# Performance work log

Measured on AMD Instinct MI355X. Metric: run time of the kernel, lower is better.

## Reference

```python
import jax, jax.numpy as jnp
import numpy as np
import math

B, N, D, K = 4, 4096, 1024, 8


def setup_inputs() -> dict:
    key = jax.random.key(0)
    ks = jax.random.split(key, 9)
    s = 0.02
    return {
        "summaries": jax.random.normal(ks[0], (B, N, D), dtype=jnp.float32),
        "Wq": jax.random.normal(ks[1], (D, D), dtype=jnp.float32) * s,
        "bq": jnp.zeros((D,), dtype=jnp.float32),
        "Wk": jax.random.normal(ks[2], (D, D), dtype=jnp.float32) * s,
        "bk": jnp.zeros((D,), dtype=jnp.float32),
        "Wv": jax.random.normal(ks[3], (D, D), dtype=jnp.float32) * s,
        "bv": jnp.zeros((D,), dtype=jnp.float32),
        "Wo": jax.random.normal(ks[4], (D, D), dtype=jnp.float32) * s,
        "bo": jnp.zeros((D,), dtype=jnp.float32),
    }


def reference(summaries, Wq, bq, Wk, bk, Wv, bv, Wo, bo):
    b_, n_, d_ = summaries.shape
    q = summaries @ Wq + bq
    k = summaries @ Wk + bk
    v = summaries @ Wv + bv
    # [B, N, N] causal scores
    scores = jnp.einsum("bnd,bmd->bnm", q, k) / math.sqrt(d_)
    causal = jnp.triu(jnp.full((n_, n_), -jnp.inf, dtype=scores.dtype), k=1)
    scores = scores + causal
    # top-k sparse attention (N > K here, matching the torch branch)
    topk_vals, topk_idx = jax.lax.top_k(scores, K)  # [B, N, K]
    bi = jnp.arange(b_)[:, None, None]
    ri = jnp.arange(n_)[None, :, None]
    sparse = jnp.full_like(scores, -jnp.inf).at[bi, ri, topk_idx].set(topk_vals)
    attn = jax.nn.softmax(sparse, axis=-1)
    out = jnp.einsum("bnm,bmd->bnd", attn, v)
    return out @ Wo + bo
```

## Files before the change

### kernel.cpp

```cpp
#include <hip/hip_runtime.h>
#include <cstdint>
#include <cstddef>

#define B_ 4
#define N_ 4096
#define D_ 1024
#define CAND 16
#define M_ (B_*N_)
#define MD_ ((size_t)M_ * D_)
#define DD_ ((size_t)D_ * D_)

typedef __attribute__((ext_vector_type(8))) short short8;
typedef __attribute__((ext_vector_type(4))) float floatx4;

__device__ __align__(16) float          g_Qf[MD_];
__device__ __align__(16) float          g_Kf[MD_];
__device__ __align__(16) unsigned short g_Qb[MD_];
__device__ __align__(16) unsigned short g_Kb[MD_];
__device__ __align__(16) float          g_Vf[MD_];
__device__ __align__(16) unsigned short g_AO[MD_];
__device__ __align__(16) unsigned short g_X0[MD_];
__device__ __align__(16) unsigned short g_X1[MD_];
__device__ __align__(16) unsigned short g_Wq0T[DD_];
__device__ __align__(16) unsigned short g_Wq1T[DD_];
__device__ __align__(16) unsigned short g_Wk0T[DD_];
__device__ __align__(16) unsigned short g_Wk1T[DD_];
__device__ __align__(16) unsigned short g_WvT[DD_];
__device__ __align__(16) unsigned short g_WoT[DD_];
__device__ __align__(16) float          g_S[(size_t)B_ * N_ * N_];
__device__ __align__(16) int            g_cand[(size_t)M_ * CAND];

__device__ __forceinline__ float b2f(unsigned short u){
  return __uint_as_float(((unsigned int)u) << 16);
}
__device__ __forceinline__ unsigned short f2b(float f){
  unsigned int b = __float_as_uint(f);
  b += 0x7fffu + ((b >> 16) & 1u);
  return (unsigned short)(b >> 16);
}
__device__ __forceinline__ void split2(float x, unsigned short& h0,
                                       unsigned short& h1){
  h0 = f2b(x);
  float r1 = x - b2f(h0);
  h1 = f2b(r1);
}

__device__ __forceinline__ void gl_lds16(const void* g, void* l){
  __builtin_amdgcn_global_load_lds(
      (const __attribute__((address_space(1))) unsigned int*)g,
      (__attribute__((address_space(3))) unsigned int*)l, 16, 0, 0);
}

__global__ __launch_bounds__(256)
void transpose2(const float* __restrict__ Wv, const float* __restrict__ Wo){
  __shared__ float tile[32][33];
  const float* src = blockIdx.z ? Wo : Wv;
  unsigned short* dst = blockIdx.z ? g_WoT : g_WvT;
  int tx = threadIdx.x, ty = threadIdx.y;
  int n0 = blockIdx.x * 32, k0 = blockIdx.y * 32;
  for (int r = ty; r < 32; r += 8) tile[r][tx] = src[(size_t)(k0 + r) * D_ + n0 + tx];
  __syncthreads();
  for (int r = ty; r < 32; r += 8) dst[(size_t)(n0 + r) * D_ + k0 + tx] = f2b(tile[tx][r]);
}

__global__ __launch_bounds__(256)
void split_wT(const float* __restrict__ Wq, const float* __restrict__ Wk){
  __shared__ float tile[32][33];
  const float* src = blockIdx.z ? Wk : Wq;
  unsigned short* d0 = blockIdx.z ? g_Wk0T : g_Wq0T;
  unsigned short* d1 = blockIdx.z ? g_Wk1T : g_Wq1T;
  int tx = threadIdx.x, ty = threadIdx.y;
  int n0 = blockIdx.x * 32, k0 = blockIdx.y * 32;
  for (int r = ty; r < 32; r += 8) tile[r][tx] = src[(size_t)(k0 + r) * D_ + n0 + tx];
  __syncthreads();
  for (int r = ty; r < 32; r += 8){
    unsigned short h0, h1;
    split2(tile[tx][r], h0, h1);
    size_t o = (size_t)(n0 + r) * D_ + k0 + tx;
    d0[o] = h0; d1[o] = h1;
  }
}

__global__ __launch_bounds__(256)
void split_x(const float* __restrict__ X){
  size_t i = ((size_t)blockIdx.x * 256 + threadIdx.x) * 4;
  if (i >= MD_) return;
  float4 x = *(const float4*)&X[i];
  ushort4 u0, u1;
  split2(x.x, u0.x, u1.x);
  split2(x.y, u0.y, u1.y);
  split2(x.z, u0.z, u1.z);
  split2(x.w, u0.w, u1.w);
  *(ushort4*)&g_X0[i] = u0;
  *(ushort4*)&g_X1[i] = u1;
}

__global__ __launch_bounds__(256, 2)
void qk_split_gemm(const float* __restrict__ bias, int which){
  int p = blockIdx.x;
  int lin = (p & 7) * 128 + (p >> 3);
  int mt = lin >> 3;
  int nt = lin & 7;

  const unsigned short* __restrict__ B0 = which ? g_Wk0T : g_Wq0T;
  const unsigned short* __restrict__ B1 = which ? g_Wk1T : g_Wq1T;
  float* __restrict__ outf = which ? g_Kf : g_Qf;
  unsigned short* __restrict__ outb = which ? g_Kb : g_Qb;

  __shared__ unsigned short __align__(16) As0[128 * 64];
  __shared__ unsigned short __align__(16) As1[128 * 64];
  __shared__ unsigned short __align__(16) Bs0[128 * 64];
  __shared__ unsigned short __align__(16) Bs1[128 * 64];

  int tid = threadIdx.x;
  size_t m0 = (size_t)mt * 128;
  int n0 = nt * 128;
  int l = tid & 63, wid = tid >> 6;
  int wm = (wid >> 1) * 64, wn = (wid & 1) * 64;
  int quad = l >> 4, lr = l & 15;

  floatx4 acc[4][4];
  #pragma unroll
  for (int i = 0; i < 4; i++)
    #pragma unroll
    for (int j = 0; j < 4; j++) acc[i][j] = (floatx4)0.0f;

  for (int k0 = 0; k0 < D_; k0 += 64){
    #pragma unroll
    for (int c = 0; c < 4; c++){
      int d = c * 4096 + tid * 16;
      int rw = d >> 7;
      int sc = ((d & 127) ^ ((rw & 7) << 4)) >> 1;
      size_t ao = (m0 + rw) * D_ + k0 + sc;
      size_t bo = (size_t)(n0 + rw) * D_ + k0 + sc;
      gl_lds16(&g_X0[ao], &As0[d >> 1]);
      gl_lds16(&g_X1[ao], &As1[d >> 1]);
      gl_lds16(&B0[bo], &Bs0[d >> 1]);
      gl_lds16(&B1[bo], &Bs1[d >> 1]);
    }
    __syncthreads();
    #pragma unroll
    for (int kk = 0; kk < 2; kk++){
      short8 a0[4], a1[4], b0[4], b1[4];
      #pragma unroll
      for (int i = 0; i < 4; i++){
        int rw = wm + i * 16 + lr;
        int byt = rw * 128 + ((kk * 64 + quad * 16) ^ ((rw & 7) << 4));
        a0[i] = *(const short8*)&As0[byt >> 1];
        a1[i] = *(const short8*)&As1[byt >> 1];
      }
      #pragma unroll
      for (int j = 0; j < 4; j++){
        int rw = wn + j * 16 + lr;
        int byt = rw * 128 + ((kk * 64 + quad * 16) ^ ((rw & 7) << 4));
        b0[j] = *(const short8*)&Bs0[byt >> 1];
        b1[j] = *(const short8*)&Bs1[byt >> 1];
      }
      #pragma unroll
      for (int i = 0; i < 4; i++)
        #pragma unroll
        for (int j = 0; j < 4; j++){
          acc[i][j] = __builtin_amdgcn_mfma_f32_16x16x32_bf16(a0[i], b1[j], acc[i][j], 0, 0, 0);
          acc[i][j] = __builtin_amdgcn_mfma_f32_16x16x32_bf16(a1[i], b0[j], acc[i][j], 0, 0, 0);
          acc[i][j] = __builtin_amdgcn_mfma_f32_16x16x32_bf16(a0[i], b0[j], acc[i][j], 0, 0, 0);
        }
    }
    __syncthreads();
  }
  #pragma unroll
  for (int i = 0; i < 4; i++)
    #pragma unroll
    for (int j = 0; j < 4; j++)
      #pragma unroll
      for (int rg = 0; rg < 4; rg++){
        size_t row = m0 + wm + i * 16 + quad * 4 + rg;
        int col = n0 + wn + j * 16 + lr;
        float val = acc[i][j][rg] + bias[col];
        outf[row * D_ + col] = val;
        outb[row * D_ + col] = f2b(val);
      }
}

__global__ __launch_bounds__(256, 2)
void gemm_bf16(const float* __restrict__ bias, float* __restrict__ Cout, int sel){
  const unsigned short* Asrc = sel ? g_AO : g_X0;
  const unsigned short* Bt = sel ? g_WoT : g_WvT;
  float* C = sel ? Cout : g_Vf;
  __shared__ unsigned short __align__(16) As[128 * 128];
  __shared__ unsigned short __align__(16) Bs[128 * 128];
  int p = blockIdx.x;
  int lin = (p & 7) * 128 + (p >> 3);
  int mt = lin >> 3;
  int nt = lin & 7;
  int tid = threadIdx.x;
  size_t m0 = (size_t)mt * 128;
  int n0 = nt * 128;
  int l = tid & 63, wid = tid >> 6;
  int wm = (wid >> 1) * 64, wn = (wid & 1) * 64;
  int quad = l >> 4, lr = l & 15;
  floatx4 acc[4][4];
  #pragma unroll
  for (int i = 0; i < 4; i++)
    #pragma unroll
    for (int j = 0; j < 4; j++) acc[i][j] = (floatx4)0.0f;

  for (int k0 = 0; k0 < D_; k0 += 128){
    #pragma unroll
    for (int c = 0; c < 8; c++){
      int d = c * 4096 + tid * 16;
      int rw = d >> 8;
      int sc = ((d & 255) ^ ((rw & 7) << 4)) >> 1;
      gl_lds16(&Asrc[(m0 + rw) * D_ + k0 + sc], &As[d >> 1]);
      gl_lds16(&Bt[(size_t)(n0 + rw) * D_ + k0 + sc], &Bs[d >> 1]);
    }
    __syncthreads();
    #pragma unroll
    for (int kk = 0; kk < 4; kk++){
      short8 af[4], bf[4];
      #pragma unroll
      for (int i = 0; i < 4; i++){
        int rw = wm + i * 16 + lr;
        int byt = rw * 256 + ((kk * 64 + quad * 16) ^ ((rw & 7) << 4));
        af[i] = *(const short8*)&As[byt >> 1];
      }
      #pragma unroll
      for (int j = 0; j < 4; j++){
        int rw = wn + j * 16 + lr;
        int byt = rw * 256 + ((kk * 64 + quad * 16) ^ ((rw & 7) << 4));
        bf[j] = *(const short8*)&Bs[byt >> 1];
      }
      #pragma unroll
      for (int i = 0; i < 4; i++)
        #pragma unroll
        for (int j = 0; j < 4; j++)
          acc[i][j] = __builtin_amdgcn_mfma_f32_16x16x32_bf16(af[i], bf[j], acc[i][j], 0, 0, 0);
    }
    __syncthreads();
  }
  #pragma unroll
  for (int i = 0; i < 4; i++)
    #pragma unroll
    for (int j = 0; j < 4; j++)
      #pragma unroll
      for (int rg = 0; rg < 4; rg++){
        size_t row = m0 + wm + i * 16 + quad * 4 + rg;
        int col = n0 + wn + j * 16 + lr;
        C[row * D_ + col] = acc[i][j][rg] + bias[col];
      }
}

__global__ __launch_bounds__(256, 2)
void scores_gemm(){
  int jt = blockIdx.x, it = blockIdx.y, b = blockIdx.z;
  if (jt > it) return;
  __shared__ unsigned short __align__(16) As[128 * 128];
  __shared__ unsigned short __align__(16) Bs[128 * 128];
  int tid = threadIdx.x;
  size_t am0 = (size_t)b * N_ + it * 128;
  size_t bn0 = (size_t)b * N_ + jt * 128;
  int l = tid & 63, wid = tid >> 6;
  int wm = (wid >> 1) * 64, wn = (wid & 1) * 64;
  int quad = l >> 4, lr = l & 15;
  floatx4 acc[4][4];
  #pragma unroll
  for (int i = 0; i < 4; i++)
    #pragma unroll
    for (int j = 0; j < 4; j++) acc[i][j] = (floatx4)0.0f;

  for (int k0 = 0; k0 < D_; k0 += 128){
    #pragma unroll
    for (int c = 0; c < 8; c++){
      int d = c * 4096 + tid * 16;
      int rw = d >> 8;
      int sc = ((d & 255) ^ ((rw & 7) << 4)) >> 1;
      gl_lds16(&g_Qb[(am0 + rw) * D_ + k0 + sc], &As[d >> 1]);
      gl_lds16(&g_Kb[(bn0 + rw) * D_ + k0 + sc], &Bs[d >> 1]);
    }
    __syncthreads();
    #pragma unroll
    for (int kk = 0; kk < 4; kk++){
      short8 af[4], bf[4];
      #pragma unroll
      for (int i = 0; i < 4; i++){
        int rw = wm + i * 16 + lr;
        int byt = rw * 256 + ((kk * 64 + quad * 16) ^ ((rw & 7) << 4));
        af[i] = *(const short8*)&As[byt >> 1];
      }
      #pragma unroll
      for (int j = 0; j < 4; j++){
        int rw = wn + j * 16 + lr;
        int byt = rw * 256 + ((kk * 64 + quad * 16) ^ ((rw & 7) << 4));
        bf[j] = *(const short8*)&Bs[byt >> 1];
      }
      #pragma unroll
      for (int i = 0; i < 4; i++)
        #pragma unroll
        for (int j = 0; j < 4; j++)
          acc[i][j] = __builtin_amdgcn_mfma_f32_16x16x32_bf16(af[i], bf[j], acc[i][j], 0, 0, 0);
    }
    __syncthreads();
  }
  #pragma unroll
  for (int i = 0; i < 4; i++)
    #pragma unroll
    for (int j = 0; j < 4; j++)
      #pragma unroll
      for (int rg = 0; rg < 4; rg++){
        int row = it * 128 + wm + i * 16 + quad * 4 + rg;
        int col = jt * 128 + wn + j * 16 + lr;
        float v = acc[i][j][rg] * 0.03125f;
        if (col > row) v = -3.0e38f;
        g_S[((size_t)b * N_ + row) * N_ + col] = v;
      }
}

__global__ __launch_bounds__(256)
void row_topk(){
  __shared__ float lv[CAND * 256];
  __shared__ int   li[CAND * 256];
  int w = threadIdx.x >> 6, l = threadIdx.x & 63;
  int g = threadIdx.x;
  int i = blockIdx.x * 4 + w;
  int irow = i & (N_ - 1);
  const float* Srow = &g_S[(size_t)i * N_];
  #pragma unroll
  for (int u = 0; u < CAND; u++){ lv[u * 256 + g] = -3.0e38f; li[u * 256 + g] = -1; }
  float vmin = -3.0e38f; int pmin = 0;
  for (int j0 = l * 4; j0 <= irow; j0 += 256){
    float4 v4 = *(const float4*)&Srow[j0];
    #pragma unroll
    for (int e = 0; e < 4; e++){
      float v = (&v4.x)[e];
      if (v > vmin){
        lv[pmin * 256 + g] = v; li[pmin * 256 + g] = j0 + e;
        float m = lv[g]; int p = 0;
        #pragma unroll
        for (int u = 1; u < CAND; u++){ float x = lv[u * 256 + g]; if (x < m){ m = x; p = u; } }
        vmin = m; pmin = p;
      }
    }
  }
  float mv = lv[g]; int mp = 0;
  #pragma unroll
  for (int u = 1; u < CAND; u++){ float x = lv[u * 256 + g]; if (x > mv){ mv = x; mp = u; } }
  int mj = li[mp * 256 + g];
  for (int rd = 0; rd < CAND; rd++){
    float bv = mv; int bj = mj; int bl = l;
    #pragma unroll
    for (int off = 32; off >= 1; off >>= 1){
      float ov = __shfl_xor(bv, off);
      int oj = __shfl_xor(bj, off);
      int ol = __shfl_xor(bl, off);
      if (ov > bv || (ov == bv && ol < bl)){ bv = ov; bj = oj; bl = ol; }
    }
    bool valid = (bv > -2.9e38f);
    if (l == 0) g_cand[(size_t)i * CAND + rd] = valid ? bj : -1;
    if (valid && bl == l){
      lv[mp * 256 + g] = -3.0e38f;
      mv = lv[g]; mp = 0;
      #pragma unroll
      for (int u = 1; u < CAND; u++){ float x = lv[u * 256 + g]; if (x > mv){ mv = x; mp = u; } }
      mj = li[mp * 256 + g];
    }
  }
}

__global__ __launch_bounds__(256)
void rescore_gather(){
  int i = blockIdx.x;
  int b = i >> 12;
  int tid = threadIdx.x, l = tid & 63, w = tid >> 6;
  __shared__ double cs[CAND];
  __shared__ int cid[CAND];
  __shared__ float ws8[8];
  __shared__ int id8[8];
  if (tid < CAND) cid[tid] = g_cand[(size_t)i * CAND + tid];
  __syncthreads();
  double q[16];
  #pragma unroll
  for (int u = 0; u < 16; u++) q[u] = (double)g_Qf[(size_t)i * D_ + l + 64 * u];
  for (int c = w * 4; c < w * 4 + 4; c++){
    int j = cid[c];
    double s = 0.0;
    if (j >= 0){
      size_t ko = ((size_t)(b * N_ + j)) * D_;
      #pragma unroll
      for (int u = 0; u < 16; u++) s = fma(q[u], (double)g_Kf[ko + l + 64 * u], s);
    }
    #pragma unroll
    for (int off = 32; off >= 1; off >>= 1) s += __shfl_down(s, off);
    if (l == 0) cs[c] = (j >= 0) ? s * 0.03125 : -1.0e300;
  }
  __syncthreads();
  if (tid == 0){
    double v8[8]; int i8[8];
    bool used[CAND];
    for (int u = 0; u < CAND; u++) used[u] = false;
    for (int rk = 0; rk < 8; rk++){
      double best = -1.0e300; int bp = -1;
      for (int c = 0; c < CAND; c++)
        if (!used[c] && cid[c] >= 0 && cs[c] > best){ best = cs[c]; bp = c; }
      if (bp >= 0){ used[bp] = true; v8[rk] = best; i8[rk] = cid[bp]; }
      else { v8[rk] = -1.0e300; i8[rk] = -1; }
    }
    if (i8[0] < 0){ i8[0] = i & (N_ - 1); v8[0] = 0.0; }
    double mx = v8[0];
    double e[8]; double Z = 0.0;
    for (int rk = 0; rk < 8; rk++){
      e[rk] = (i8[rk] >= 0) ? exp(v8[rk] - mx) : 0.0;
      Z += e[rk];
    }
    for (int rk = 0; rk < 8; rk++){
      id8[rk] = i8[rk];
      ws8[rk] = (float)(e[rk] / Z);
    }
  }
  __syncthreads();
  int d0 = tid * 4;
  float a0 = 0.f, a1 = 0.f, a2 = 0.f, a3 = 0.f;
  #pragma unroll
  for (int rk = 0; rk < 8; rk++){
    int j = id8[rk];
    if (j < 0) continue;
    float wgt = ws8[rk];
    float4 vv = *(const float4*)&g_Vf[((size_t)(b * N_ + j)) * D_ + d0];
    a0 += wgt * vv.x; a1 += wgt * vv.y; a2 += wgt * vv.z; a3 += wgt * vv.w;
  }
  ushort4 o;
  o.x = f2b(a0); o.y = f2b(a1); o.z = f2b(a2); o.w = f2b(a3);
  *(ushort4*)&g_AO[(size_t)i * D_ + d0] = o;
}

extern "C" void kernel_launch(void* const* d_in, const int* in_sizes, int n_in,
                              void* d_out, int out_size, void* d_ws, size_t ws_size,
                              hipStream_t stream){
  const float* S  = (const float*)d_in[0];
  const float* Wq = (const float*)d_in[1];
  const float* bq = (const float*)d_in[2];
  const float* Wk = (const float*)d_in[3];
  const float* bk = (const float*)d_in[4];
  const float* Wv = (const float*)d_in[5];
  const float* bv = (const float*)d_in[6];
  const float* Wo = (const float*)d_in[7];
  const float* bo = (const float*)d_in[8];
  float* out = (float*)d_out;
  (void)d_ws; (void)ws_size; (void)in_sizes; (void)n_in; (void)out_size;

  transpose2<<<dim3(32, 32, 2), dim3(32, 8), 0, stream>>>(Wv, Wo);
  split_wT<<<dim3(32, 32, 2), dim3(32, 8), 0, stream>>>(Wq, Wk);
  split_x<<<dim3(M_), 256, 0, stream>>>(S);
  qk_split_gemm<<<dim3(1024), 256, 0, stream>>>(bq, 0);
  qk_split_gemm<<<dim3(1024), 256, 0, stream>>>(bk, 1);
  gemm_bf16<<<dim3(1024), 256, 0, stream>>>(bv, nullptr, 0);
  scores_gemm<<<dim3(32, 32, 4), 256, 0, stream>>>();
  row_topk<<<dim3(M_ / 4), 256, 0, stream>>>();
  rescore_gather<<<dim3(M_), 256, 0, stream>>>();
  gemm_bf16<<<dim3(1024), 256, 0, stream>>>(bo, out, 1);
}
```

Measured before the change: 1.104 ms.

## Merge Q/K GEMM launches, shrink candidate set, rescore in fp32

Merges the separate Q and K split-precision GEMM launches into one 2048-block launch, so the Q and K tiles for the same row block are scheduled close together and share the X tiles in cache. Cuts the top-k candidate count from 16 to 12, which shrinks the row_topk selection work and the rescoring gathers. The rescore dot products and the softmax move from double to float, with three independent accumulators per wave. The smaller candidate margin and fp32 rescoring raise the risk of picking a different top-8 set when scores are close.

```diff
diff --git a/kernel.cpp b/kernel.cpp
--- a/kernel.cpp
+++ b/kernel.cpp
@@ -5,7 +5,7 @@
 #define B_ 4
 #define N_ 4096
 #define D_ 1024
-#define CAND 16
+#define CAND 12
 #define M_ (B_*N_)
 #define MD_ ((size_t)M_ * D_)
 #define DD_ ((size_t)D_ * D_)
@@ -96,14 +96,17 @@
 }
 
 __global__ __launch_bounds__(256, 2)
-void qk_split_gemm(const float* __restrict__ bias, int which){
+void qk_split_gemm(const float* __restrict__ bq, const float* __restrict__ bk){
   int p = blockIdx.x;
-  int lin = (p & 7) * 128 + (p >> 3);
-  int mt = lin >> 3;
-  int nt = lin & 7;
+  int lin = (p & 7) * 256 + (p >> 3);
+  int mt = lin >> 4;
+  int sub = lin & 15;
+  int which = sub >> 3;
+  int nt = sub & 7;
 
   const unsigned short* __restrict__ B0 = which ? g_Wk0T : g_Wq0T;
   const unsigned short* __restrict__ B1 = which ? g_Wk1T : g_Wq1T;
+  const float* __restrict__ bias = which ? bk : bq;
   float* __restrict__ outf = which ? g_Kf : g_Qf;
   unsigned short* __restrict__ outb = which ? g_Kb : g_Qb;
 
@@ -370,49 +373,65 @@
   int i = blockIdx.x;
   int b = i >> 12;
   int tid = threadIdx.x, l = tid & 63, w = tid >> 6;
-  __shared__ double cs[CAND];
+  __shared__ float cs[CAND];
   __shared__ int cid[CAND];
   __shared__ float ws8[8];
   __shared__ int id8[8];
   if (tid < CAND) cid[tid] = g_cand[(size_t)i * CAND + tid];
   __syncthreads();
-  double q[16];
-  #pragma unroll
-  for (int u = 0; u < 16; u++) q[u] = (double)g_Qf[(size_t)i * D_ + l + 64 * u];
-  for (int c = w * 4; c < w * 4 + 4; c++){
-    int j = cid[c];
-    double s = 0.0;
-    if (j >= 0){
-      size_t ko = ((size_t)(b * N_ + j)) * D_;
-      #pragma unroll
-      for (int u = 0; u < 16; u++) s = fma(q[u], (double)g_Kf[ko + l + 64 * u], s);
-    }
-    #pragma unroll
-    for (int off = 32; off >= 1; off >>= 1) s += __shfl_down(s, off);
-    if (l == 0) cs[c] = (j >= 0) ? s * 0.03125 : -1.0e300;
+  float q[16];
+  #pragma unroll
+  for (int u = 0; u < 16; u++) q[u] = g_Qf[(size_t)i * D_ + l + 64 * u];
+  {
+    int c0 = w * 3;
+    int j0 = cid[c0], j1 = cid[c0 + 1], j2 = cid[c0 + 2];
+    size_t k0o = ((size_t)(b * N_ + (j0 < 0 ? 0 : j0))) * D_;
+    size_t k1o = ((size_t)(b * N_ + (j1 < 0 ? 0 : j1))) * D_;
+    size_t k2o = ((size_t)(b * N_ + (j2 < 0 ? 0 : j2))) * D_;
+    float a0 = 0.f, a1 = 0.f, a2 = 0.f;
+    #pragma unroll
+    for (int u = 0; u < 16; u++){
+      float k0v = g_Kf[k0o + l + 64 * u];
+      float k1v = g_Kf[k1o + l + 64 * u];
+      float k2v = g_Kf[k2o + l + 64 * u];
+      a0 = fmaf(q[u], k0v, a0);
+      a1 = fmaf(q[u], k1v, a1);
+      a2 = fmaf(q[u], k2v, a2);
+    }
+    #pragma unroll
+    for (int off = 32; off >= 1; off >>= 1){
+      a0 += __shfl_down(a0, off);
+      a1 += __shfl_down(a1, off);
+      a2 += __shfl_down(a2, off);
+    }
+    if (l == 0){
+      cs[c0]     = (j0 >= 0) ? a0 * 0.03125f : -3.0e38f;
+      cs[c0 + 1] = (j1 >= 0) ? a1 * 0.03125f : -3.0e38f;
+      cs[c0 + 2] = (j2 >= 0) ? a2 * 0.03125f : -3.0e38f;
+    }
   }
   __syncthreads();
   if (tid == 0){
-    double v8[8]; int i8[8];
+    float v8[8]; int i8[8];
     bool used[CAND];
     for (int u = 0; u < CAND; u++) used[u] = false;
     for (int rk = 0; rk < 8; rk++){
-      double best = -1.0e300; int bp = -1;
+      float best = -3.0e38f; int bp = -1;
       for (int c = 0; c < CAND; c++)
         if (!used[c] && cid[c] >= 0 && cs[c] > best){ best = cs[c]; bp = c; }
       if (bp >= 0){ used[bp] = true; v8[rk] = best; i8[rk] = cid[bp]; }
-      else { v8[rk] = -1.0e300; i8[rk] = -1; }
-    }
-    if (i8[0] < 0){ i8[0] = i & (N_ - 1); v8[0] = 0.0; }
-    double mx = v8[0];
-    double e[8]; double Z = 0.0;
+      else { v8[rk] = -3.0e38f; i8[rk] = -1; }
+    }
+    if (i8[0] < 0){ i8[0] = i & (N_ - 1); v8[0] = 0.0f; }
+    float mx = v8[0];
+    float e[8]; float Z = 0.0f;
     for (int rk = 0; rk < 8; rk++){
-      e[rk] = (i8[rk] >= 0) ? exp(v8[rk] - mx) : 0.0;
+      e[rk] = (i8[rk] >= 0) ? expf(v8[rk] - mx) : 0.0f;
       Z += e[rk];
     }
     for (int rk = 0; rk < 8; rk++){
       id8[rk] = i8[rk];
-      ws8[rk] = (float)(e[rk] / Z);
+      ws8[rk] = e[rk] / Z;
     }
   }
   __syncthreads();
@@ -449,8 +468,7 @@
   transpose2<<<dim3(32, 32, 2), dim3(32, 8), 0, stream>>>(Wv, Wo);
   split_wT<<<dim3(32, 32, 2), dim3(32, 8), 0, stream>>>(Wq, Wk);
   split_x<<<dim3(M_), 256, 0, stream>>>(S);
-  qk_split_gemm<<<dim3(1024), 256, 0, stream>>>(bq, 0);
-  qk_split_gemm<<<dim3(1024), 256, 0, stream>>>(bk, 1);
+  qk_split_gemm<<<dim3(2048), 256, 0, stream>>>(bq, bk);
   gemm_bf16<<<dim3(1024), 256, 0, stream>>>(bv, nullptr, 0);
   scores_gemm<<<dim3(32, 32, 4), 256, 0, stream>>>();
   row_topk<<<dim3(M_ / 4), 256, 0, stream>>>();
```

Result: faster. 963.3 us (-12.8%).
